# Performance work log

Hardware: AMD Instinct MI355X
Metric: run time of the kernel (lower is better)

The kernel has to match this reference:

```python
import jax, jax.numpy as jnp
import numpy as np

B, N, N_FEAT = 16, 1024, 128
N_LAYER, AGG_HIDDEN, FC_HIDDEN, N_CLASS = 3, 64, 128, 10
NEG_INF = -9e15
LEAKY_SLOPE = 0.2


def setup_inputs() -> dict:
    key = jax.random.key(0)
    ks = jax.random.split(key, 8)
    x = jax.random.normal(ks[0], (B, N, N_FEAT), dtype=jnp.float32)
    adj = jax.random.randint(ks[1], (B, N, N), 0, 2).astype(jnp.float32)
    # per-layer GAT params, stacked over layers
    Ws = jax.random.normal(ks[2], (N_LAYER, N_FEAT, AGG_HIDDEN), dtype=jnp.float32) * 0.1
    a1 = jax.random.normal(ks[3], (N_LAYER, AGG_HIDDEN), dtype=jnp.float32) * 0.1
    a2 = jax.random.normal(ks[4], (N_LAYER, AGG_HIDDEN), dtype=jnp.float32) * 0.1
    W1 = jax.random.normal(ks[5], (AGG_HIDDEN * N_LAYER, FC_HIDDEN), dtype=jnp.float32) * 0.05
    b1 = jnp.zeros((FC_HIDDEN,), dtype=jnp.float32)
    W2 = jax.random.normal(ks[6], (FC_HIDDEN, N_CLASS), dtype=jnp.float32) * 0.05
    b2 = jnp.zeros((N_CLASS,), dtype=jnp.float32)
    return {"x": x, "adj": adj, "Ws": Ws, "a1": a1, "a2": a2,
            "W1": W1, "b1": b1, "W2": W2, "b2": b2}


def _gat_layer(x, adj, W, a1, a2):
    # h: [B, N, H]
    h = jnp.einsum('bnf,fh->bnh', x, W)
    # e_ij = LeakyReLU(a1.h_i + a2.h_j)  -- split-a trick, avoids [B,N,N,2H]
    f1 = jnp.einsum('bnh,h->bn', h, a1)
    f2 = jnp.einsum('bnh,h->bn', h, a2)
    e = jax.nn.leaky_relu(f1[:, :, None] + f2[:, None, :], LEAKY_SLOPE)  # [B,N,N]
    att = jax.nn.softmax(jnp.where(adj > 0, e, NEG_INF), axis=-1)
    return jnp.einsum('bnm,bmh->bnh', att, h)


def reference(x, adj, Ws, a1, a2, W1, b1, W2, b2):
    # eval mode: dropout is identity
    outs = [jax.nn.relu(_gat_layer(x, adj, Ws[i], a1[i], a2[i]))
            for i in range(N_LAYER)]
    h = jnp.concatenate(outs, axis=2)          # [B, N, H*L]
    pooled = jnp.mean(h, axis=1)               # 'avg' pool over nodes -> [B, H*L]
    z = jax.nn.relu(pooled @ W1 + b1)
    return jax.nn.softmax(z @ W2 + b2, axis=-1)  # [B, n_class]
```

## Files before the change

kernel.cpp:

```cpp
#include <hip/hip_runtime.h>

#define B 16
#define N 1024
#define NF 128
#define NL 3
#define AH 64
#define HC 192
#define FCH 128
#define NC 10
#define L2E 1.44269504088896f

typedef __attribute__((ext_vector_type(8))) short bf16x8;
typedef __attribute__((ext_vector_type(4))) float f32x4;
typedef __attribute__((ext_vector_type(4))) unsigned int u32x4;

static __device__ __forceinline__ unsigned short f2bf(float f) {
  unsigned int x = __builtin_bit_cast(unsigned int, f);
  return (unsigned short)((x + 0x7fffu + ((x >> 16) & 1u)) >> 16);
}
static __device__ __forceinline__ float bf2f(unsigned short u) {
  unsigned int x = ((unsigned int)u) << 16;
  return __builtin_bit_cast(float, x);
}

__global__ __launch_bounds__(256) void k_mask(
    const float* __restrict__ adj, unsigned short* __restrict__ mskf)
{
  __shared__ unsigned short sm[16][66];
  const int t = threadIdx.x;
  const int stripe = blockIdx.x;
  const float* ap = adj + (size_t)stripe * 16 * N;

  #pragma unroll
  for (int c = 0; c < 4; ++c) {
    const int row = c * 4 + (t >> 6);
    const int j0 = (t & 63) * 16;
    const float* p = ap + (size_t)row * N + j0;
    unsigned int bits = 0;
    #pragma unroll
    for (int q = 0; q < 4; ++q) {
      const uint4 u = *(const uint4*)(p + q * 4);
      bits |= (u.x ? 1u : 0u) << (q * 4 + 0);
      bits |= (u.y ? 1u : 0u) << (q * 4 + 1);
      bits |= (u.z ? 1u : 0u) << (q * 4 + 2);
      bits |= (u.w ? 1u : 0u) << (q * 4 + 3);
    }
    sm[row][t & 63] = (unsigned short)bits;
  }
  __syncthreads();

  #pragma unroll
  for (int cc = 0; cc < 4; ++cc) {
    const int o = cc * 256 + t;
    const int jt = o >> 6, lane_o = o & 63;
    const int lr = lane_o & 15, lg = lane_o >> 4;
    const int sh = (lg & 1) * 8;
    const unsigned int b0 = (sm[lr][jt * 4 + (lg >> 1)] >> sh) & 0xffu;
    const unsigned int b1 = (sm[lr][jt * 4 + 2 + (lg >> 1)] >> sh) & 0xffu;
    mskf[(size_t)stripe * 1024 + o] = (unsigned short)(b0 | (b1 << 8));
  }
}

__global__ __launch_bounds__(256, 2) void k_feat(
    const float* __restrict__ x, const float* __restrict__ Ws,
    const float* __restrict__ a1, const float* __restrict__ a2,
    unsigned short* __restrict__ h_f, float* __restrict__ f1g,
    float* __restrict__ f2g)
{
  __shared__ float xs[64][132];
  __shared__ unsigned short wl[2][64][136];
  unsigned short (*hlds)[72] = (unsigned short(*)[72])&xs[0][0];
  const int t = threadIdx.x;
  const int n0g = blockIdx.x * 64;
  const int gb = n0g >> 10, nl0 = n0g & 1023;
  const int wv = t >> 6, lane = t & 63;
  const int lr = lane & 15, lg = lane >> 4;
  const int lrow = wv * 16 + lr;
  const int wcol = t & 63, woct = t >> 6;

#define LOADW(R, L) {                                                         \
    _Pragma("unroll")                                                         \
    for (int p = 0; p < 4; ++p) {                                             \
      const int oct = p * 4 + woct;                                           \
      _Pragma("unroll")                                                       \
      for (int i = 0; i < 8; ++i)                                             \
        R[p][i] = Ws[((size_t)(L) * NF + oct * 8 + i) * AH + wcol];           \
    } }
#define WRITEW(R) {                                                           \
    _Pragma("unroll")                                                         \
    for (int p = 0; p < 4; ++p) {                                             \
      const int oct = p * 4 + woct;                                           \
      bf16x8 hv, lv;                                                          \
      _Pragma("unroll")                                                       \
      for (int i = 0; i < 8; ++i) {                                           \
        const unsigned short hi = f2bf(R[p][i]);                              \
        hv[i] = (short)hi;                                                    \
        lv[i] = (short)f2bf(R[p][i] - bf2f(hi));                              \
      }                                                                       \
      *(bf16x8*)&wl[0][wcol][oct * 8] = hv;                                   \
      *(bf16x8*)&wl[1][wcol][oct * 8] = lv;                                   \
    } }
#define MFMAL(L) {                                                            \
    _Pragma("unroll")                                                         \
    for (int n2 = 0; n2 < 4; ++n2) {                                          \
      const int n = (L) * 4 + n2;                                             \
      _Pragma("unroll")                                                       \
      for (int kf = 0; kf < 4; ++kf) {                                        \
        const bf16x8 whi = *(const bf16x8*)&wl[0][n2 * 16 + lr][kf * 32 + lg * 8]; \
        const bf16x8 wlo = *(const bf16x8*)&wl[1][n2 * 16 + lr][kf * 32 + lg * 8]; \
        acc[n] = __builtin_amdgcn_mfma_f32_16x16x32_bf16(xhi[kf], whi, acc[n], 0, 0, 0); \
        acc[n] = __builtin_amdgcn_mfma_f32_16x16x32_bf16(xhi[kf], wlo, acc[n], 0, 0, 0); \
        acc[n] = __builtin_amdgcn_mfma_f32_16x16x32_bf16(xlo[kf], whi, acc[n], 0, 0, 0); \
      }                                                                       \
    } }

  float wrA[4][8], wrB[4][8];
  LOADW(wrA, 0);

  #pragma unroll
  for (int p = 0; p < 8; ++p) {
    const int q = p * 256 + t;
    const int row = q >> 5, c4 = (q & 31) * 4;
    *(float4*)&xs[row][c4] = *(const float4*)&x[(size_t)(n0g + row) * NF + c4];
  }
  __syncthreads();

  bf16x8 xhi[4], xlo[4];
  #pragma unroll
  for (int kf = 0; kf < 4; ++kf) {
    const float4 q0 = *(const float4*)&xs[lrow][kf * 32 + lg * 8];
    const float4 q1 = *(const float4*)&xs[lrow][kf * 32 + lg * 8 + 4];
    const float xv[8] = {q0.x, q0.y, q0.z, q0.w, q1.x, q1.y, q1.z, q1.w};
    #pragma unroll
    for (int e = 0; e < 8; ++e) {
      const unsigned short hi = f2bf(xv[e]);
      xhi[kf][e] = (short)hi;
      xlo[kf][e] = (short)f2bf(xv[e] - bf2f(hi));
    }
  }

  f32x4 acc[12];
  #pragma unroll
  for (int n = 0; n < 12; ++n) acc[n] = (f32x4){0.f, 0.f, 0.f, 0.f};

  WRITEW(wrA);
  LOADW(wrB, 1);
  __syncthreads();
  MFMAL(0);
  __syncthreads();
  WRITEW(wrB);
  LOADW(wrA, 2);
  __syncthreads();
  MFMAL(1);
  __syncthreads();
  WRITEW(wrA);
  __syncthreads();
  MFMAL(2);

#undef LOADW
#undef WRITEW
#undef MFMAL

  float s1[3][4], s2[3][4];
  #pragma unroll
  for (int l = 0; l < 3; ++l)
    #pragma unroll
    for (int r = 0; r < 4; ++r) { s1[l][r] = 0.f; s2[l][r] = 0.f; }
  #pragma unroll
  for (int n = 0; n < 12; ++n) {
    const int col = n * 16 + lr;
    const float a1v = a1[col] * L2E, a2v = a2[col] * L2E;
    const int l = n >> 2;
    #pragma unroll
    for (int r = 0; r < 4; ++r) {
      s1[l][r] += acc[n][r] * a1v;
      s2[l][r] += acc[n][r] * a2v;
    }
  }
  #pragma unroll
  for (int off = 1; off < 16; off <<= 1)
    #pragma unroll
    for (int l = 0; l < 3; ++l)
      #pragma unroll
      for (int r = 0; r < 4; ++r) {
        s1[l][r] += __shfl_xor(s1[l][r], off);
        s2[l][r] += __shfl_xor(s2[l][r], off);
      }
  if (lr == 0) {
    #pragma unroll
    for (int l = 0; l < 3; ++l)
      #pragma unroll
      for (int r = 0; r < 4; ++r) {
        const int rw = n0g + wv * 16 + lg * 4 + r;
        f1g[(size_t)l * (B * N) + rw] = s1[l][r];
        f2g[(size_t)l * (B * N) + rw] = s2[l][r];
      }
  }

  __syncthreads();
  #pragma unroll
  for (int n = 0; n < 12; ++n) {
    const int col = n * 16 + lr;
    #pragma unroll
    for (int rp = 0; rp < 2; ++rp) {
      const unsigned int pr = (unsigned int)f2bf(acc[n][rp * 2]) |
                              ((unsigned int)f2bf(acc[n][rp * 2 + 1]) << 16);
      *(unsigned int*)&hlds[col][wv * 16 + lg * 4 + rp * 2] = pr;
    }
  }
  __syncthreads();
  #pragma unroll
  for (int p = 0; p < 6; ++p) {
    const int widx = p * 256 + t;
    const int lane_w = widx & 63;
    const int jb2 = (widx >> 6) & 1;
    const int n_w = (widx >> 7) & 3;
    const int l_w = widx >> 9;
    const int col = l_w * 64 + n_w * 16 + (lane_w & 15);
    const int jloc = jb2 * 32 + (lane_w >> 4) * 8;
    const size_t off =
        ((((size_t)(gb * 3 + l_w) * 4 + n_w) * 32 + (nl0 >> 5) + jb2) * 64 + lane_w) * 8;
    *(uint4*)&h_f[off] = *(const uint4*)&hlds[col][jloc];
  }
}

__global__ __launch_bounds__(192, 3) void k_att(
    const unsigned short* __restrict__ mskf, const unsigned short* __restrict__ h_f,
    const float* __restrict__ f1, const float* __restrict__ f2,
    float* __restrict__ pooled)
{
  const int bid = blockIdx.x;
  const int blk = (bid & 7) * 128 + (bid >> 3);
  const int b = blk >> 6;
  const int i0 = (blk & 63) * 16;
  const int ph = ((bid * 5) & 7) * 128;
  const int t = threadIdx.x;
  const int l = t >> 6, lane = t & 63;
  const int lr = lane & 15, lg = lane >> 4;

  __shared__ float uvt[NL][2][N];

  const float* f2p = f2 + (size_t)l * (B * N) + b * N;
  float mx = -1e30f;
  #pragma unroll
  for (int ch = 0; ch < 4; ++ch) {
    const int jb = ch * 256 + lane * 4;
    const float4 q = *(const float4*)&f2p[jb];
    mx = fmaxf(mx, fmaxf(fmaxf(q.x, q.y), fmaxf(q.z, q.w)));
    *(float4*)&uvt[l][0][jb] =
        (float4){exp2f(q.x), exp2f(q.y), exp2f(q.z), exp2f(q.w)};
    *(float4*)&uvt[l][1][jb] =
        (float4){exp2f(0.2f * q.x), exp2f(0.2f * q.y), exp2f(0.2f * q.z), exp2f(0.2f * q.w)};
  }
  #pragma unroll
  for (int off = 1; off < 64; off <<= 1) mx = fmaxf(mx, __shfl_xor(mx, off));

  const float f1r = f1[(size_t)l * (B * N) + b * N + i0 + lr];
  const float tts = f1r + mx;
  const float sr = fmaxf(tts, 0.f) + 0.2f * fminf(tts, 0.f);
  const float A = exp2f(f1r - sr);
  const float C = exp2f(0.2f * f1r - sr);

  const unsigned short* hfb = h_f + ((size_t)(b * 3 + l)) * 65536;
  const unsigned short* mrow = mskf + ((size_t)(b * 64 + (i0 >> 4))) * 1024;
  const float* ut = &uvt[l][0][0];
  const float* vt = &uvt[l][1][0];
  const bf16x8 ones = {(short)0x3F80, (short)0x3F80, (short)0x3F80, (short)0x3F80,
                       (short)0x3F80, (short)0x3F80, (short)0x3F80, (short)0x3F80};

  f32x4 acc[4];
  #pragma unroll
  for (int n = 0; n < 4; ++n) acc[n] = (f32x4){0.f, 0.f, 0.f, 0.f};
  f32x4 accd = (f32x4){0.f, 0.f, 0.f, 0.f};

#define LOADJ(BUF, MW, J) {                                                   \
    const int jj = (J) & (N - 1);                                             \
    MW = (unsigned int)mrow[(jj >> 6) * 64 + lane];                           \
    _Pragma("unroll")                                                         \
    for (int q = 0; q < 8; ++q) {                                             \
      const int ks = q >> 2, n = q & 3;                                       \
      BUF[q] = *(const bf16x8*)&hfb[(((size_t)n * 32 + (jj >> 5) + ks) * 64 + \
                                     lane) * 8];                              \
    } }

#define COMPJ(BUF, MW, J) {                                                   \
    _Pragma("unroll")                                                         \
    for (int ks = 0; ks < 2; ++ks) {                                          \
      const int kb = ((J) & (N - 1)) + ks * 32 + lg * 8;                      \
      const float4 u0 = *(const float4*)&ut[kb];                              \
      const float4 u1 = *(const float4*)&ut[kb + 4];                          \
      const float4 v0 = *(const float4*)&vt[kb];                              \
      const float4 v1 = *(const float4*)&vt[kb + 4];                          \
      const unsigned int mby = ((MW) >> (ks * 8)) & 0xffu;                    \
      const float uu[8] = {u0.x, u0.y, u0.z, u0.w, u1.x, u1.y, u1.z, u1.w};   \
      const float vv[8] = {v0.x, v0.y, v0.z, v0.w, v1.x, v1.y, v1.z, v1.w};   \
      unsigned int pk[4];                                                     \
      _Pragma("unroll")                                                       \
      for (int ep = 0; ep < 4; ++ep) {                                        \
        unsigned int pr[2];                                                   \
        _Pragma("unroll")                                                     \
        for (int h = 0; h < 2; ++h) {                                         \
          const int e = ep * 2 + h;                                           \
                  \
          const float p = fmaxf(A * uu[e], C * vv[e]);                        \
                  \
          const unsigned int sel =                                            \
              (unsigned int)(((int)(mby << (31 - e))) >> 31);                 \
          pr[h] = (__builtin_bit_cast(unsigned int, p) + 0x8000u) & sel;      \
        }                                                                     \
        pk[ep] = __builtin_amdgcn_perm(pr[1], pr[0], 0x07060302u);            \
      }                                                                       \
      const u32x4 pkv = {pk[0], pk[1], pk[2], pk[3]};                         \
      const bf16x8 av = __builtin_bit_cast(bf16x8, pkv);                      \
      _Pragma("unroll")                                                       \
      for (int n = 0; n < 4; ++n)                                             \
        acc[n] = __builtin_amdgcn_mfma_f32_16x16x32_bf16(av, BUF[ks * 4 + n], \
                                                         acc[n], 0, 0, 0);    \
      accd = __builtin_amdgcn_mfma_f32_16x16x32_bf16(av, ones, accd, 0, 0, 0);\
    } }

#define SBAR __builtin_amdgcn_sched_barrier(0)

  bf16x8 bA[8], bB[8];
  unsigned int mwA, mwB;
  LOADJ(bA, mwA, ph);
  SBAR;
  for (int j0 = 0; j0 < N; j0 += 128) {
    LOADJ(bB, mwB, ph + j0 + 64);
    SBAR;
    COMPJ(bA, mwA, ph + j0);
    SBAR;
    LOADJ(bA, mwA, ph + j0 + 128);
    SBAR;
    COMPJ(bB, mwB, ph + j0 + 64);
    SBAR;
  }
#undef LOADJ
#undef COMPJ
#undef SBAR

  float dn[4];
  #pragma unroll
  for (int r = 0; r < 4; ++r) dn[r] = 1.f / fmaxf(accd[r], 1e-37f);

  #pragma unroll
  for (int n = 0; n < 4; ++n) {
    float csum = 0.f;
    #pragma unroll
    for (int r = 0; r < 4; ++r) csum += fmaxf(acc[n][r] * dn[r], 0.f);
    csum += __shfl_xor(csum, 16);
    csum += __shfl_xor(csum, 32);
    if (lg == 0) atomicAdd(&pooled[b * HC + l * 64 + n * 16 + lr], csum);
  }
}

__global__ __launch_bounds__(192) void k_head(
    const float* __restrict__ pooled_sums, const float* __restrict__ W1,
    const float* __restrict__ b1, const float* __restrict__ W2,
    const float* __restrict__ b2, float* __restrict__ out)
{
  const int b = blockIdx.x, t = threadIdx.x;
  __shared__ float pooled[HC];
  __shared__ float z[FCH];
  __shared__ float logits[NC];

  if (t < HC) pooled[t] = pooled_sums[b * HC + t] * (1.f / (float)N);
  __syncthreads();

  if (t < FCH) {
    float a = b1[t];
    #pragma unroll 4
    for (int f = 0; f < HC; ++f) a += pooled[f] * W1[(size_t)f * FCH + t];
    z[t] = a > 0.f ? a : 0.f;
  }
  __syncthreads();

  if (t < NC) {
    float a = b2[t];
    #pragma unroll 4
    for (int f = 0; f < FCH; ++f) a += z[f] * W2[(size_t)f * NC + t];
    logits[t] = a;
  }
  __syncthreads();

  if (t == 0) {
    float mxl = logits[0];
    for (int c = 1; c < NC; ++c) mxl = fmaxf(mxl, logits[c]);
    float e[NC], sum = 0.f;
    for (int c = 0; c < NC; ++c) { e[c] = __expf(logits[c] - mxl); sum += e[c]; }
    const float inv = 1.f / sum;
    for (int c = 0; c < NC; ++c) out[b * NC + c] = e[c] * inv;
  }
}

extern "C" void kernel_launch(void* const* d_in, const int* in_sizes, int n_in,
                              void* d_out, int out_size, void* d_ws, size_t ws_size,
                              hipStream_t stream)
{
  const float* x   = (const float*)d_in[0];
  const float* adj = (const float*)d_in[1];
  const float* Ws  = (const float*)d_in[2];
  const float* a1  = (const float*)d_in[3];
  const float* a2  = (const float*)d_in[4];
  const float* W1  = (const float*)d_in[5];
  const float* b1  = (const float*)d_in[6];
  const float* W2  = (const float*)d_in[7];
  const float* b2  = (const float*)d_in[8];
  float* out = (float*)d_out;

  unsigned short* h_f   = (unsigned short*)d_ws;
  float*          f1    = (float*)(h_f + (size_t)B * HC * N);
  float*          f2    = f1 + (size_t)NL * B * N;
  float*          pooled= f2 + (size_t)NL * B * N;
  unsigned short* mskf  = (unsigned short*)(pooled + B * HC + 16);

  hipMemsetAsync(pooled, 0, (size_t)B * HC * sizeof(float), stream);
  k_mask<<<B * 64, 256, 0, stream>>>(adj, mskf);
  k_feat<<<256, 256, 0, stream>>>(x, Ws, a1, a2, h_f, f1, f2);
  k_att <<<1024, 192, 0, stream>>>(mskf, h_f, f1, f2, pooled);
  k_head<<<B, 192, 0, stream>>>(pooled, W1, b1, W2, b2, out);
}
```

Before: 74.78 us.

## Fuse adjacency mask packing into attention kernel and drop memset

Removes the separate mask-packing kernel: each attention block now reads its 16-row adjacency stripe, packs it into bits in shared memory, and builds the MFMA mask words from LDS. The pooled-buffer zeroing moves into the first block of the feature kernel, which removes the memset launch. Together these cut two launches and a round trip through global memory for the packed mask. In exchange, the adjacency read now sits at the start of the attention kernel behind a barrier, where it is not overlapped with other work, and it adds shared memory per block.

New measurement: 69.97 us. -6.4%, faster.

```diff
diff --git a/kernel.cpp b/kernel.cpp
--- a/kernel.cpp
+++ b/kernel.cpp
@@ -23,49 +23,11 @@
   return __builtin_bit_cast(float, x);
 }
 
-__global__ __launch_bounds__(256) void k_mask(
-    const float* __restrict__ adj, unsigned short* __restrict__ mskf)
-{
-  __shared__ unsigned short sm[16][66];
-  const int t = threadIdx.x;
-  const int stripe = blockIdx.x;
-  const float* ap = adj + (size_t)stripe * 16 * N;
-
-  #pragma unroll
-  for (int c = 0; c < 4; ++c) {
-    const int row = c * 4 + (t >> 6);
-    const int j0 = (t & 63) * 16;
-    const float* p = ap + (size_t)row * N + j0;
-    unsigned int bits = 0;
-    #pragma unroll
-    for (int q = 0; q < 4; ++q) {
-      const uint4 u = *(const uint4*)(p + q * 4);
-      bits |= (u.x ? 1u : 0u) << (q * 4 + 0);
-      bits |= (u.y ? 1u : 0u) << (q * 4 + 1);
-      bits |= (u.z ? 1u : 0u) << (q * 4 + 2);
-      bits |= (u.w ? 1u : 0u) << (q * 4 + 3);
-    }
-    sm[row][t & 63] = (unsigned short)bits;
-  }
-  __syncthreads();
-
-  #pragma unroll
-  for (int cc = 0; cc < 4; ++cc) {
-    const int o = cc * 256 + t;
-    const int jt = o >> 6, lane_o = o & 63;
-    const int lr = lane_o & 15, lg = lane_o >> 4;
-    const int sh = (lg & 1) * 8;
-    const unsigned int b0 = (sm[lr][jt * 4 + (lg >> 1)] >> sh) & 0xffu;
-    const unsigned int b1 = (sm[lr][jt * 4 + 2 + (lg >> 1)] >> sh) & 0xffu;
-    mskf[(size_t)stripe * 1024 + o] = (unsigned short)(b0 | (b1 << 8));
-  }
-}
-
 __global__ __launch_bounds__(256, 2) void k_feat(
     const float* __restrict__ x, const float* __restrict__ Ws,
     const float* __restrict__ a1, const float* __restrict__ a2,
     unsigned short* __restrict__ h_f, float* __restrict__ f1g,
-    float* __restrict__ f2g)
+    float* __restrict__ f2g, float* __restrict__ pooled)
 {
   __shared__ float xs[64][132];
   __shared__ unsigned short wl[2][64][136];
@@ -77,6 +39,11 @@
   const int lr = lane & 15, lg = lane >> 4;
   const int lrow = wv * 16 + lr;
   const int wcol = t & 63, woct = t >> 6;
+
+  if (blockIdx.x == 0) {
+    #pragma unroll
+    for (int i = 0; i < 12; ++i) pooled[i * 256 + t] = 0.f;
+  }
 
 #define LOADW(R, L) {                                                         \
     _Pragma("unroll")                                                         \
@@ -225,7 +192,7 @@
 }
 
 __global__ __launch_bounds__(192, 3) void k_att(
-    const unsigned short* __restrict__ mskf, const unsigned short* __restrict__ h_f,
+    const float* __restrict__ adj, const unsigned short* __restrict__ h_f,
     const float* __restrict__ f1, const float* __restrict__ f2,
     float* __restrict__ pooled)
 {
@@ -237,8 +204,26 @@
   const int t = threadIdx.x;
   const int l = t >> 6, lane = t & 63;
   const int lr = lane & 15, lg = lane >> 4;
+  const int msh = (lg & 1) * 8;
 
   __shared__ float uvt[NL][2][N];
+  __shared__ unsigned short sm[16][66];
+
+  const float* ap = adj + ((size_t)(b * N + i0)) * N;
+  for (int q = t; q < 1024; q += 192) {
+    const int row = q >> 6, ch = q & 63;
+    const float* p = ap + (size_t)row * N + ch * 16;
+    unsigned int bits = 0;
+    #pragma unroll
+    for (int qq = 0; qq < 4; ++qq) {
+      const uint4 u = *(const uint4*)(p + qq * 4);
+      bits |= (u.x ? 1u : 0u) << (qq * 4 + 0);
+      bits |= (u.y ? 1u : 0u) << (qq * 4 + 1);
+      bits |= (u.z ? 1u : 0u) << (qq * 4 + 2);
+      bits |= (u.w ? 1u : 0u) << (qq * 4 + 3);
+    }
+    sm[row][ch] = (unsigned short)bits;
+  }
 
   const float* f2p = f2 + (size_t)l * (B * N) + b * N;
   float mx = -1e30f;
@@ -262,7 +247,6 @@
   const float C = exp2f(0.2f * f1r - sr);
 
   const unsigned short* hfb = h_f + ((size_t)(b * 3 + l)) * 65536;
-  const unsigned short* mrow = mskf + ((size_t)(b * 64 + (i0 >> 4))) * 1024;
   const float* ut = &uvt[l][0][0];
   const float* vt = &uvt[l][1][0];
   const bf16x8 ones = {(short)0x3F80, (short)0x3F80, (short)0x3F80, (short)0x3F80,
@@ -273,9 +257,14 @@
   for (int n = 0; n < 4; ++n) acc[n] = (f32x4){0.f, 0.f, 0.f, 0.f};
   f32x4 accd = (f32x4){0.f, 0.f, 0.f, 0.f};
 
+  __syncthreads();
+
 #define LOADJ(BUF, MW, J) {                                                   \
     const int jj = (J) & (N - 1);                                             \
-    MW = (unsigned int)mrow[(jj >> 6) * 64 + lane];                           \
+    const int jt = jj >> 6;                                                   \
+    const unsigned int s0 = sm[lr][jt * 4 + (lg >> 1)];                       \
+    const unsigned int s1 = sm[lr][jt * 4 + 2 + (lg >> 1)];                   \
+    MW = ((s0 >> msh) & 0xffu) | (((s1 >> msh) & 0xffu) << 8);                \
     _Pragma("unroll")                                                         \
     for (int q = 0; q < 8; ++q) {                                             \
       const int ks = q >> 2, n = q & 3;                                       \
@@ -303,7 +292,6 @@
           const int e = ep * 2 + h;                                           \
                   \
           const float p = fmaxf(A * uu[e], C * vv[e]);                        \
-                  \
           const unsigned int sel =                                            \
               (unsigned int)(((int)(mby << (31 - e))) >> 31);                 \
           pr[h] = (__builtin_bit_cast(unsigned int, p) + 0x8000u) & sel;      \
@@ -412,11 +400,8 @@
   float*          f1    = (float*)(h_f + (size_t)B * HC * N);
   float*          f2    = f1 + (size_t)NL * B * N;
   float*          pooled= f2 + (size_t)NL * B * N;
-  unsigned short* mskf  = (unsigned short*)(pooled + B * HC + 16);
-
-  hipMemsetAsync(pooled, 0, (size_t)B * HC * sizeof(float), stream);
-  k_mask<<<B * 64, 256, 0, stream>>>(adj, mskf);
-  k_feat<<<256, 256, 0, stream>>>(x, Ws, a1, a2, h_f, f1, f2);
-  k_att <<<1024, 192, 0, stream>>>(mskf, h_f, f1, f2, pooled);
+
+  k_feat<<<256, 256, 0, stream>>>(x, Ws, a1, a2, h_f, f1, f2, pooled);
+  k_att <<<1024, 192, 0, stream>>>(adj, h_f, f1, f2, pooled);
   k_head<<<B, 192, 0, stream>>>(pooled, W1, b1, W2, b2, out);
 }
```
